# Performance work log

Hardware: AMD Instinct MI355X
Metric: run time of the kernel (lower is better)

## Reference

```python
import jax, jax.numpy as jnp
import numpy as np

L, D, DM, H, FF = 2048, 32, 1024, 16, 4096
DH = DM // H  # 64
SCALE = float(np.sqrt(DH))


def layernorm(x, g, b, eps=1e-5):
    mu = jnp.mean(x, axis=-1, keepdims=True)
    var = jnp.mean(jnp.square(x - mu), axis=-1, keepdims=True)
    return (x - mu) * jax.lax.rsqrt(var + eps) * g + b


def setup_inputs() -> dict:
    key = jax.random.key(0)
    ks = jax.random.split(key, 8)
    p = lambda k, shp: jax.random.normal(k, shp, jnp.float32) * 0.02
    return {
        "src": jax.random.normal(ks[0], (L, DM), jnp.float32),
        "target": jax.random.normal(ks[1], (L, D, DM), jnp.float32),
        "attn_mask": jnp.zeros((L, D), jnp.float32),
        "Wq": p(ks[2], (DM, DM)), "bq": jnp.zeros((DM,), jnp.float32),
        "Wk": p(ks[3], (DM, DM)), "bk": jnp.zeros((DM,), jnp.float32),
        "Wv": p(ks[4], (DM, DM)), "bv": jnp.zeros((DM,), jnp.float32),
        "W1": p(ks[5], (DM, FF)), "b1": jnp.zeros((FF,), jnp.float32),
        "W2": p(ks[6], (FF, DM)), "b2": jnp.zeros((DM,), jnp.float32),
        "g1": jnp.ones((DM,), jnp.float32), "beta1": jnp.zeros((DM,), jnp.float32),
        "g2": jnp.ones((DM,), jnp.float32), "beta2": jnp.zeros((DM,), jnp.float32),
    }


def reference(src, target, attn_mask, Wq, bq, Wk, bk, Wv, bv,
              W1, b1, W2, b2, g1, beta1, g2, beta2):
    # projections: src (L, DM), target (L, D, DM)
    q = (src @ Wq + bq).reshape(L, H, DH)            # (L, H, DH)
    k = (target @ Wk + bk).reshape(L, D, H, DH)       # (L, D, H, DH)
    v = (target @ Wv + bv).reshape(L, D, H, DH)
    # per-position attention over the D candidates: scores (H, L, D)
    scores = jnp.einsum('lhd,lkhd->hlk', q, k) / SCALE
    scores = scores + attn_mask[None, :, :]
    probs = jax.nn.softmax(scores, axis=-1)
    ctx = jnp.einsum('hlk,lkhd->lhd', probs, v).reshape(L, DM)
    x = layernorm(src + ctx, g1, beta1)
    ff = jax.nn.gelu(x @ W1 + b1, approximate=False) @ W2 + b2
    return layernorm(x + ff, g2, beta2)
```

## Files before the change

kernel.cpp:

```cpp
#include <hip/hip_runtime.h>
#include <hip/hip_bf16.h>

#define L  2048
#define D  32
#define DM 1024
#define H  16
#define DH 64
#define FF 4096

typedef unsigned short u16;
typedef __attribute__((ext_vector_type(8))) short bf16x8;
typedef __attribute__((ext_vector_type(4))) float f32x4;
typedef __attribute__((ext_vector_type(4))) unsigned int u32x4;
typedef __attribute__((ext_vector_type(8))) unsigned short u16x8;
typedef __attribute__((ext_vector_type(4))) unsigned short u16x4;

static __device__ __forceinline__ u16 f2bf(float f) {
    union { __hip_bfloat16 b; u16 u; } cv;
    cv.b = __float2bfloat16(f);
    return cv.u;
}
static __device__ __forceinline__ void gll16(const u16* gsrc, u16* ldst) {
    __builtin_amdgcn_global_load_lds(
        (const __attribute__((address_space(1))) unsigned int*)gsrc,
        (__attribute__((address_space(3))) unsigned int*)ldst, 16, 0, 0);
}

__global__ __launch_bounds__(256) void prep_bf(const float* __restrict__ a, u16* __restrict__ oa,
                                               const float* __restrict__ b, u16* __restrict__ ob) {
    const int i = blockIdx.x * 256 + threadIdx.x;
    const int na4 = (L * DM) / 4;
    const float* in;  u16* out;  int j;
    if (i < na4) { in = a; out = oa; j = i; }
    else         { in = b; out = ob; j = i - na4; }
    const float4 v = reinterpret_cast<const float4*>(in)[j];
    u16x4 o = { f2bf(v.x), f2bf(v.y), f2bf(v.z), f2bf(v.w) };
    *reinterpret_cast<u16x4*>(out + (long)j * 4) = o;
}

__global__ void prep_T(const float* __restrict__ Wq, u16* __restrict__ oWq,
                       const float* __restrict__ Wv, u16* __restrict__ oWv,
                       const float* __restrict__ W1, u16* __restrict__ oW1,
                       const float* __restrict__ W2, u16* __restrict__ oW2) {
    __shared__ float tile[32][33];
    const int b = blockIdx.x;
    const float* in; u16* out; int R, C, bx, by;
    if (b < 1024)      { in = Wq; out = oWq; R = DM; C = DM; int bb = b;        bx = (bb & 31) * 32;  by = (bb >> 5) * 32; }
    else if (b < 2048) { in = Wv; out = oWv; R = DM; C = DM; int bb = b - 1024; bx = (bb & 31) * 32;  by = (bb >> 5) * 32; }
    else if (b < 6144) { in = W1; out = oW1; R = DM; C = FF; int bb = b - 2048; bx = (bb & 127) * 32; by = (bb >> 7) * 32; }
    else               { in = W2; out = oW2; R = FF; C = DM; int bb = b - 6144; bx = (bb & 31) * 32;  by = (bb >> 5) * 32; }
    const int tx = threadIdx.x, ty = threadIdx.y;
    #pragma unroll
    for (int i = 0; i < 32; i += 8)
        tile[ty + i][tx] = in[(long)(by + ty + i) * C + bx + tx];
    __syncthreads();
    #pragma unroll
    for (int i = 0; i < 32; i += 8)
        out[(long)(bx + ty + i) * R + by + tx] = f2bf(tile[tx][ty + i]);
}

template<int EPI, int BN>
__global__ __launch_bounds__(256) void gemm128(
    const u16* __restrict__ A, int lda, long aZ,
    const u16* __restrict__ Bt, int ldb, long bZ,
    void* __restrict__ Cv, int ldc, long cZ,
    const float* __restrict__ bias, int biasZ, int K)
{
    constexpr int NI = BN / 32;
    __shared__ u16 As[128 * 64];
    __shared__ u16 Bs[BN * 64];
    const int t = threadIdx.x, lane = t & 63, w = t >> 6;
    const int z = blockIdx.z;
    const int nxy = gridDim.x * gridDim.y;
    int fid = blockIdx.y * gridDim.x + blockIdx.x;
    const int q8 = nxy >> 3;
    fid = (fid & 7) * q8 + (fid >> 3);
    const int bx = fid % gridDim.x, by = fid / gridDim.x;
    const int mBase = by * 128, nBase = bx * BN;
    const u16* Ab = A + (long)z * aZ;
    const u16* Bb = Bt + (long)z * bZ;
    const int wr = w >> 1, wc = w & 1;
    const int sr = lane >> 3, sg = lane & 7, sswz = sg ^ sr;
    f32x4 acc[4][NI];
    #pragma unroll
    for (int mi = 0; mi < 4; ++mi)
        #pragma unroll
        for (int ni = 0; ni < NI; ++ni) acc[mi][ni] = (f32x4){0.f, 0.f, 0.f, 0.f};

    for (int k0 = 0; k0 < K; k0 += 64) {
        #pragma unroll
        for (int i = 0; i < 4; ++i) {
            const int r = w * 32 + i * 8 + sr;
            gll16(&Ab[(long)(mBase + r) * lda + k0 + sswz * 8], &As[r * 64 + sg * 8]);
        }
        #pragma unroll
        for (int i = 0; i < NI; ++i) {
            const int r = w * (BN / 4) + i * 8 + sr;
            gll16(&Bb[(long)(nBase + r) * ldb + k0 + sswz * 8], &Bs[r * 64 + sg * 8]);
        }
        __syncthreads();
        #pragma unroll
        for (int ks = 0; ks < 2; ++ks) {
            bf16x8 aF[4], bF[NI];
            #pragma unroll
            for (int mi = 0; mi < 4; ++mi) {
                const int rr = wr * 64 + mi * 16 + (lane & 15);
                aF[mi] = *reinterpret_cast<const bf16x8*>(
                    &As[rr * 64 + ((ks * 4 + (lane >> 4)) ^ (rr & 7)) * 8]);
            }
            #pragma unroll
            for (int ni = 0; ni < NI; ++ni) {
                const int rr = wc * (BN / 2) + ni * 16 + (lane & 15);
                bF[ni] = *reinterpret_cast<const bf16x8*>(
                    &Bs[rr * 64 + ((ks * 4 + (lane >> 4)) ^ (rr & 7)) * 8]);
            }
            #pragma unroll
            for (int mi = 0; mi < 4; ++mi)
                #pragma unroll
                for (int ni = 0; ni < NI; ++ni)
                    acc[mi][ni] = __builtin_amdgcn_mfma_f32_16x16x32_bf16(
                        aF[mi], bF[ni], acc[mi][ni], 0, 0, 0);
        }
        __syncthreads();
    }
    const int rb = mBase + wr * 64 + ((lane >> 4) << 2);
    const int cb = nBase + wc * (BN / 2) + (lane & 15);
    #pragma unroll
    for (int mi = 0; mi < 4; ++mi) {
        #pragma unroll
        for (int ni = 0; ni < NI; ++ni) {
            const int col = cb + ni * 16;
            const float badd = bias ? bias[(long)z * biasZ + col] : 0.f;
            #pragma unroll
            for (int i = 0; i < 4; ++i) {
                float v = acc[mi][ni][i] + badd;
                if (EPI == 2) v = 0.5f * v * (1.f + erff(v * 0.70710678118654752f));
                const long off = (long)z * cZ + (long)(rb + mi * 16 + i) * ldc + col;
                if (EPI == 1) reinterpret_cast<float*>(Cv)[off] = v;
                else          reinterpret_cast<u16*>(Cv)[off]  = f2bf(v);
            }
        }
    }
}

#define NLV5 8
__global__ __launch_bounds__(512, 2) void attn_v5(
    const u16* __restrict__ qk,
    const float* __restrict__ target,
    const float* __restrict__ mask,
    u16* __restrict__ tw)
{
    extern __shared__ u16 smem[];
    u16*   tgtS0 = smem;
    u16*   tgtS1 = smem + D * DM;
    f32x4* red   = (f32x4*)(smem + 2 * D * DM);

    const int t = threadIdx.x, lane = t & 63, w = t >> 6;
    const int g = lane >> 4, hm = lane & 15;
    const int l0 = blockIdx.x * NLV5;

    float4 pf[16];
    bf16x8 qc[2][4];
    {
        const float* tl = target + (long)l0 * (D * DM);
        #pragma unroll
        for (int it = 0; it < 16; ++it)
            pf[it] = reinterpret_cast<const float4*>(tl)[it * 512 + t];
        #pragma unroll
        for (int it = 0; it < 16; ++it) {
            const int i = it * 512 + t;
            const int d = i >> 8, mm = (i & 255) * 4, cc = mm ^ ((d & 15) << 3);
            u16x4 o = { f2bf(pf[it].x), f2bf(pf[it].y), f2bf(pf[it].z), f2bf(pf[it].w) };
            *reinterpret_cast<u16x4*>(&tgtS0[d * DM + cc]) = o;
        }
        const float* tn = target + (long)(l0 + 1) * (D * DM);
        #pragma unroll
        for (int it = 0; it < 16; ++it)
            pf[it] = reinterpret_cast<const float4*>(tn)[it * 512 + t];
        const u16* qb = qk + (long)l0 * (H * DM) + hm * DM + w * 128 + g * 8;
        #pragma unroll
        for (int ks = 0; ks < 4; ++ks)
            qc[0][ks] = *reinterpret_cast<const bf16x8*>(&qb[ks * 32]);
    }
    __syncthreads();

    #pragma unroll
    for (int li = 0; li < NLV5; ++li) {
        const int l = l0 + li;
        const int cur = li & 1, nxt = cur ^ 1;
        u16* curS = cur ? tgtS1 : tgtS0;
        u16* nxtS = cur ? tgtS0 : tgtS1;

        const float* mrow = mask + (long)l * D;
        float mk[8];
        #pragma unroll
        for (int r = 0; r < 4; ++r) { mk[r] = mrow[4 * g + r]; mk[4 + r] = mrow[16 + 4 * g + r]; }

        if (li < NLV5 - 1) {
            #pragma unroll
            for (int it = 0; it < 16; ++it) {
                const int i = it * 512 + t;
                const int d = i >> 8, mm = (i & 255) * 4, cc = mm ^ ((d & 15) << 3);
                u16x4 o = { f2bf(pf[it].x), f2bf(pf[it].y), f2bf(pf[it].z), f2bf(pf[it].w) };
                *reinterpret_cast<u16x4*>(&nxtS[d * DM + cc]) = o;
            }
            if (li < NLV5 - 2) {
                const float* tn = target + (long)(l + 2) * (D * DM);
                #pragma unroll
                for (int it = 0; it < 16; ++it)
                    pf[it] = reinterpret_cast<const float4*>(tn)[it * 512 + t];
            }
            const u16* qn = qk + (long)(l + 1) * (H * DM) + hm * DM + w * 128 + g * 8;
            #pragma unroll
            for (int ks = 0; ks < 4; ++ks)
                qc[nxt][ks] = *reinterpret_cast<const bf16x8*>(&qn[ks * 32]);
        }

        f32x4 a0 = {0.f, 0.f, 0.f, 0.f}, a1 = {0.f, 0.f, 0.f, 0.f};
        const int swz = hm << 3;
        #pragma unroll
        for (int ks = 0; ks < 4; ++ks) {
            const int mcol = w * 128 + ks * 32 + g * 8;
            const bf16x8 x0 = *reinterpret_cast<const bf16x8*>(&curS[hm * DM + (mcol ^ swz)]);
            const bf16x8 x1 = *reinterpret_cast<const bf16x8*>(&curS[(16 + hm) * DM + (mcol ^ swz)]);
            a0 = __builtin_amdgcn_mfma_f32_16x16x32_bf16(x0, qc[cur][ks], a0, 0, 0, 0);
            a1 = __builtin_amdgcn_mfma_f32_16x16x32_bf16(x1, qc[cur][ks], a1, 0, 0, 0);
        }
        red[(w * 2 + 0) * 64 + lane] = a0;
        red[(w * 2 + 1) * 64 + lane] = a1;
        __syncthreads();

        f32x4 s0 = red[lane], s1 = red[64 + lane];
        #pragma unroll
        for (int ww = 1; ww < 8; ++ww) {
            s0 += red[(ww * 2 + 0) * 64 + lane];
            s1 += red[(ww * 2 + 1) * 64 + lane];
        }

        float sc[8];
        #pragma unroll
        for (int r = 0; r < 4; ++r) {
            sc[r]     = s0[r] * 0.125f + mk[r];
            sc[4 + r] = s1[r] * 0.125f + mk[4 + r];
        }
        float mx = sc[0];
        #pragma unroll
        for (int r = 1; r < 8; ++r) mx = fmaxf(mx, sc[r]);
        mx = fmaxf(mx, __shfl_xor(mx, 16));
        mx = fmaxf(mx, __shfl_xor(mx, 32));
        float sum = 0.f;
        #pragma unroll
        for (int r = 0; r < 8; ++r) { sc[r] = __expf(sc[r] - mx); sum += sc[r]; }
        sum += __shfl_xor(sum, 16);
        sum += __shfl_xor(sum, 32);
        const float pinv = 1.0f / sum;
        bf16x8 pfrag;
        #pragma unroll
        for (int r = 0; r < 8; ++r) pfrag[r] = (short)f2bf(sc[r] * pinv);

        u16* twl = tw + (long)l * (H * DM);
        const f32x4 zero = {0.f, 0.f, 0.f, 0.f};
        #pragma unroll
        for (int i = 0; i < 8; ++i) {
            const int mg = w * 8 + i;
            const int m = mg * 16 + hm;
            bf16x8 af;
            #pragma unroll
            for (int j = 0; j < 4; ++j) {
                const int d0 = 4 * g + j;
                const int d1 = 16 + 4 * g + j;
                af[j]     = (short)curS[d0 * DM + (m ^ (d0 << 3))];
                af[4 + j] = (short)curS[d1 * DM + (m ^ (d0 << 3))];
            }
            const f32x4 c = __builtin_amdgcn_mfma_f32_16x16x32_bf16(af, pfrag, zero, 0, 0, 0);
            u16x4 o = { f2bf(c[0]), f2bf(c[1]), f2bf(c[2]), f2bf(c[3]) };
            *reinterpret_cast<u16x4*>(&twl[hm * DM + mg * 16 + 4 * g]) = o;
        }
        __syncthreads();
    }
}

__global__ __launch_bounds__(256) void ln_fuse(
    const float* __restrict__ a, const float* __restrict__ zb, int nz, long zstride,
    const float* __restrict__ bvec,
    const float* __restrict__ g, const float* __restrict__ be,
    float* __restrict__ o32, u16* __restrict__ o16)
{
    const int l = blockIdx.x, t = threadIdx.x;
    __shared__ float S[4], SS[4];
    __shared__ float stats[2];
    const float4 va = reinterpret_cast<const float4*>(a + (long)l * DM)[t];
    float v[4] = { va.x, va.y, va.z, va.w };
    for (int zi = 0; zi < nz; ++zi) {
        const float4 q = reinterpret_cast<const float4*>(zb + (long)zi * zstride + (long)l * DM)[t];
        v[0] += q.x; v[1] += q.y; v[2] += q.z; v[3] += q.w;
    }
    if (bvec) {
        const float4 vv = reinterpret_cast<const float4*>(bvec)[t];
        v[0] += vv.x; v[1] += vv.y; v[2] += vv.z; v[3] += vv.w;
    }
    float s  = v[0] + v[1] + v[2] + v[3];
    float ss = v[0]*v[0] + v[1]*v[1] + v[2]*v[2] + v[3]*v[3];
    #pragma unroll
    for (int off = 32; off; off >>= 1) { s += __shfl_down(s, off); ss += __shfl_down(ss, off); }
    if ((t & 63) == 0) { S[t >> 6] = s; SS[t >> 6] = ss; }
    __syncthreads();
    if (t == 0) {
        const float St  = S[0] + S[1] + S[2] + S[3];
        const float SSt = SS[0] + SS[1] + SS[2] + SS[3];
        const float mu  = St * (1.f / DM);
        const float var = fmaxf(SSt * (1.f / DM) - mu * mu, 0.f);
        stats[0] = mu;
        stats[1] = rsqrtf(var + 1e-5f);
    }
    __syncthreads();
    const float mu = stats[0], rs = stats[1];
    const int c0 = t * 4;
    float ov[4];
    #pragma unroll
    for (int j = 0; j < 4; ++j) ov[j] = (v[j] - mu) * rs * g[c0 + j] + be[c0 + j];
    float4 o; o.x = ov[0]; o.y = ov[1]; o.z = ov[2]; o.w = ov[3];
    reinterpret_cast<float4*>(o32 + (long)l * DM)[t] = o;
    if (o16) {
        u16x4 q = { f2bf(ov[0]), f2bf(ov[1]), f2bf(ov[2]), f2bf(ov[3]) };
        *reinterpret_cast<u16x4*>(o16 + (long)l * DM + c0) = q;
    }
}

extern "C" void kernel_launch(void* const* d_in, const int* in_sizes, int n_in,
                              void* d_out, int out_size, void* d_ws, size_t ws_size,
                              hipStream_t stream)
{
    const float* src    = (const float*)d_in[0];
    const float* target = (const float*)d_in[1];
    const float* amask  = (const float*)d_in[2];
    const float* Wq = (const float*)d_in[3];
    const float* bq = (const float*)d_in[4];
    const float* Wk = (const float*)d_in[5];
    const float* Wv = (const float*)d_in[7];
    const float* bv = (const float*)d_in[8];
    const float* W1 = (const float*)d_in[9];
    const float* b1 = (const float*)d_in[10];
    const float* W2 = (const float*)d_in[11];
    const float* b2 = (const float*)d_in[12];
    const float* g1  = (const float*)d_in[13];
    const float* be1 = (const float*)d_in[14];
    const float* g2  = (const float*)d_in[15];
    const float* be2 = (const float*)d_in[16];

    char* ws = (char*)d_ws;
    const size_t MB = (size_t)1 << 20;
    u16*   src16 = (u16*)  (ws +  0 * MB);
    u16*   Wk16  = (u16*)  (ws +  4 * MB);
    u16*   WqT   = (u16*)  (ws +  6 * MB);
    u16*   WvT   = (u16*)  (ws +  8 * MB);
    u16*   W1T   = (u16*)  (ws + 10 * MB);
    u16*   W2T   = (u16*)  (ws + 18 * MB);
    u16*   Q16   = (u16*)  (ws + 26 * MB);
    u16*   qk16  = (u16*)  (ws + 30 * MB);
    u16*   Y16   = (u16*)  (ws + 30 * MB);
    float* ctx32 = (float*)(ws + 54 * MB);
    float* x32   = (float*)(ws + 62 * MB);
    u16*   x16   = (u16*)  (ws + 70 * MB);
    u16*   tw16  = (u16*)  (ws + 94 * MB);
    float* Z32   = (float*)(ws + 94 * MB);

    prep_bf<<<3072, 256, 0, stream>>>(src, src16, Wk, Wk16);
    prep_T<<<10240, dim3(32, 8), 0, stream>>>(Wq, WqT, Wv, WvT, W1, W1T, W2, W2T);

    gemm128<0, 64><<<dim3(DM / 64, L / 128, 1), 256, 0, stream>>>(
        src16, DM, 0, WqT, DM, 0, Q16, DM, 0, bq, 0, DM);
    gemm128<0, 128><<<dim3(DM / 128, L / 128, H), 256, 0, stream>>>(
        Q16, DM, DH, Wk16, DM, DH, qk16, H * DM, DM, nullptr, 0, DH);

    (void)hipFuncSetAttribute(reinterpret_cast<const void*>(&attn_v5),
                              hipFuncAttributeMaxDynamicSharedMemorySize, 144 * 1024);
    attn_v5<<<L / NLV5, 512, 144 * 1024, stream>>>(qk16, target, amask, tw16);

    gemm128<1, 64><<<dim3(1, L / 128, H), 256, 0, stream>>>(
        tw16, H * DM, DM, WvT, DM, (long)DH * DM, ctx32, DM, DH, bv, DH, DM);
    ln_fuse<<<L, 256, 0, stream>>>(src, ctx32, 1, 0, nullptr, g1, be1, x32, x16);
    gemm128<2, 128><<<dim3(FF / 128, L / 128, 1), 256, 0, stream>>>(
        x16, DM, 0, W1T, DM, 0, Y16, FF, 0, b1, 0, DM);
    gemm128<1, 128><<<dim3(DM / 128, L / 128, 4), 256, 0, stream>>>(
        Y16, FF, 1024, W2T, FF, 1024, Z32, DM, (long)L * DM, nullptr, 0, 1024);
    ln_fuse<<<L, 256, 0, stream>>>(x32, Z32, 4, (long)L * DM, b2, g2, be2, (float*)d_out, nullptr);
}
```

Measured before the change: 250.8 us.

## Double-buffer GEMM LDS tiles, add MFMA priority, merge prep kernels

Adds an optional double-buffered LDS path to the bf16 GEMM. The next K tile is loaded via global_load_lds while the current tile feeds MFMAs, so one barrier per iteration replaces two. It also raises wave priority around the MFMA block and fuses the two weight/activation conversion kernels into one launch. The price is doubled LDS per block, which may lower occupancy. The pipelined path relies on a single barrier to order the async LDS writes against reads of the other buffer.

```diff
diff --git a/kernel.cpp b/kernel.cpp
--- a/kernel.cpp
+++ b/kernel.cpp
@@ -26,30 +26,33 @@
         (__attribute__((address_space(3))) unsigned int*)ldst, 16, 0, 0);
 }
 
-__global__ __launch_bounds__(256) void prep_bf(const float* __restrict__ a, u16* __restrict__ oa,
-                                               const float* __restrict__ b, u16* __restrict__ ob) {
-    const int i = blockIdx.x * 256 + threadIdx.x;
-    const int na4 = (L * DM) / 4;
-    const float* in;  u16* out;  int j;
-    if (i < na4) { in = a; out = oa; j = i; }
-    else         { in = b; out = ob; j = i - na4; }
-    const float4 v = reinterpret_cast<const float4*>(in)[j];
-    u16x4 o = { f2bf(v.x), f2bf(v.y), f2bf(v.z), f2bf(v.w) };
-    *reinterpret_cast<u16x4*>(out + (long)j * 4) = o;
-}
-
-__global__ void prep_T(const float* __restrict__ Wq, u16* __restrict__ oWq,
-                       const float* __restrict__ Wv, u16* __restrict__ oWv,
-                       const float* __restrict__ W1, u16* __restrict__ oW1,
-                       const float* __restrict__ W2, u16* __restrict__ oW2) {
+__global__ __launch_bounds__(256) void prep_all(
+    const float* __restrict__ src, u16* __restrict__ osrc,
+    const float* __restrict__ Wk,  u16* __restrict__ oWk,
+    const float* __restrict__ Wq,  u16* __restrict__ oWq,
+    const float* __restrict__ Wv,  u16* __restrict__ oWv,
+    const float* __restrict__ W1,  u16* __restrict__ oW1,
+    const float* __restrict__ W2,  u16* __restrict__ oW2)
+{
+    const int b = blockIdx.x, t = threadIdx.x;
+    if (b >= 10240) {
+        const int i = (b - 10240) * 256 + t;
+        const int na4 = (L * DM) / 4;
+        const float* in;  u16* out;  int j;
+        if (i < na4) { in = src; out = osrc; j = i; }
+        else         { in = Wk;  out = oWk;  j = i - na4; }
+        const float4 v = reinterpret_cast<const float4*>(in)[j];
+        u16x4 o = { f2bf(v.x), f2bf(v.y), f2bf(v.z), f2bf(v.w) };
+        *reinterpret_cast<u16x4*>(out + (long)j * 4) = o;
+        return;
+    }
     __shared__ float tile[32][33];
-    const int b = blockIdx.x;
     const float* in; u16* out; int R, C, bx, by;
     if (b < 1024)      { in = Wq; out = oWq; R = DM; C = DM; int bb = b;        bx = (bb & 31) * 32;  by = (bb >> 5) * 32; }
     else if (b < 2048) { in = Wv; out = oWv; R = DM; C = DM; int bb = b - 1024; bx = (bb & 31) * 32;  by = (bb >> 5) * 32; }
     else if (b < 6144) { in = W1; out = oW1; R = DM; C = FF; int bb = b - 2048; bx = (bb & 127) * 32; by = (bb >> 7) * 32; }
     else               { in = W2; out = oW2; R = FF; C = DM; int bb = b - 6144; bx = (bb & 31) * 32;  by = (bb >> 5) * 32; }
-    const int tx = threadIdx.x, ty = threadIdx.y;
+    const int tx = t & 31, ty = t >> 5;
     #pragma unroll
     for (int i = 0; i < 32; i += 8)
         tile[ty + i][tx] = in[(long)(by + ty + i) * C + bx + tx];
@@ -59,7 +62,7 @@
         out[(long)(bx + ty + i) * R + by + tx] = f2bf(tile[tx][ty + i]);
 }
 
-template<int EPI, int BN>
+template<int EPI, int BN, int PIPE>
 __global__ __launch_bounds__(256) void gemm128(
     const u16* __restrict__ A, int lda, long aZ,
     const u16* __restrict__ Bt, int ldb, long bZ,
@@ -67,8 +70,9 @@
     const float* __restrict__ bias, int biasZ, int K)
 {
     constexpr int NI = BN / 32;
-    __shared__ u16 As[128 * 64];
-    __shared__ u16 Bs[BN * 64];
+    constexpr int ASZ = 128 * 64, BSZ = BN * 64;
+    __shared__ u16 As[(PIPE ? 2 : 1) * ASZ];
+    __shared__ u16 Bs[(PIPE ? 2 : 1) * BSZ];
     const int t = threadIdx.x, lane = t & 63, w = t >> 6;
     const int z = blockIdx.z;
     const int nxy = gridDim.x * gridDim.y;
@@ -87,18 +91,34 @@
         #pragma unroll
         for (int ni = 0; ni < NI; ++ni) acc[mi][ni] = (f32x4){0.f, 0.f, 0.f, 0.f};
 
-    for (int k0 = 0; k0 < K; k0 += 64) {
+    auto STAGE = [&](int buf, int k0) {
+        u16* Ad = As + buf * ASZ;
+        u16* Bd = Bs + buf * BSZ;
         #pragma unroll
         for (int i = 0; i < 4; ++i) {
             const int r = w * 32 + i * 8 + sr;
-            gll16(&Ab[(long)(mBase + r) * lda + k0 + sswz * 8], &As[r * 64 + sg * 8]);
+            gll16(&Ab[(long)(mBase + r) * lda + k0 + sswz * 8], &Ad[r * 64 + sg * 8]);
         }
         #pragma unroll
         for (int i = 0; i < NI; ++i) {
             const int r = w * (BN / 4) + i * 8 + sr;
-            gll16(&Bb[(long)(nBase + r) * ldb + k0 + sswz * 8], &Bs[r * 64 + sg * 8]);
-        }
-        __syncthreads();
+            gll16(&Bb[(long)(nBase + r) * ldb + k0 + sswz * 8], &Bd[r * 64 + sg * 8]);
+        }
+    };
+
+    if (PIPE) { STAGE(0, 0); }
+    int cur = 0;
+    for (int k0 = 0; k0 < K; k0 += 64) {
+        if (!PIPE) {
+            STAGE(0, k0);
+            __syncthreads();
+        } else {
+            __syncthreads();
+            if (k0 + 64 < K) STAGE(cur ^ 1, k0 + 64);
+        }
+        const u16* Ar = As + cur * ASZ;
+        const u16* Br = Bs + cur * BSZ;
+        __builtin_amdgcn_s_setprio(1);
         #pragma unroll
         for (int ks = 0; ks < 2; ++ks) {
             bf16x8 aF[4], bF[NI];
@@ -106,13 +126,13 @@
             for (int mi = 0; mi < 4; ++mi) {
                 const int rr = wr * 64 + mi * 16 + (lane & 15);
                 aF[mi] = *reinterpret_cast<const bf16x8*>(
-                    &As[rr * 64 + ((ks * 4 + (lane >> 4)) ^ (rr & 7)) * 8]);
+                    &Ar[rr * 64 + ((ks * 4 + (lane >> 4)) ^ (rr & 7)) * 8]);
             }
             #pragma unroll
             for (int ni = 0; ni < NI; ++ni) {
                 const int rr = wc * (BN / 2) + ni * 16 + (lane & 15);
                 bF[ni] = *reinterpret_cast<const bf16x8*>(
-                    &Bs[rr * 64 + ((ks * 4 + (lane >> 4)) ^ (rr & 7)) * 8]);
+                    &Br[rr * 64 + ((ks * 4 + (lane >> 4)) ^ (rr & 7)) * 8]);
             }
             #pragma unroll
             for (int mi = 0; mi < 4; ++mi)
@@ -121,7 +141,9 @@
                     acc[mi][ni] = __builtin_amdgcn_mfma_f32_16x16x32_bf16(
                         aF[mi], bF[ni], acc[mi][ni], 0, 0, 0);
         }
-        __syncthreads();
+        __builtin_amdgcn_s_setprio(0);
+        if (!PIPE) __syncthreads();
+        if (PIPE) cur ^= 1;
     }
     const int rb = mBase + wr * 64 + ((lane >> 4) << 2);
     const int cb = nBase + wc * (BN / 2) + (lane & 15);
@@ -365,24 +387,24 @@
     u16*   tw16  = (u16*)  (ws + 94 * MB);
     float* Z32   = (float*)(ws + 94 * MB);
 
-    prep_bf<<<3072, 256, 0, stream>>>(src, src16, Wk, Wk16);
-    prep_T<<<10240, dim3(32, 8), 0, stream>>>(Wq, WqT, Wv, WvT, W1, W1T, W2, W2T);
-
-    gemm128<0, 64><<<dim3(DM / 64, L / 128, 1), 256, 0, stream>>>(
+    prep_all<<<13312, 256, 0, stream>>>(src, src16, Wk, Wk16,
+                                        Wq, WqT, Wv, WvT, W1, W1T, W2, W2T);
+
+    gemm128<0, 64, 1><<<dim3(DM / 64, L / 128, 1), 256, 0, stream>>>(
         src16, DM, 0, WqT, DM, 0, Q16, DM, 0, bq, 0, DM);
-    gemm128<0, 128><<<dim3(DM / 128, L / 128, H), 256, 0, stream>>>(
+    gemm128<0, 128, 0><<<dim3(DM / 128, L / 128, H), 256, 0, stream>>>(
         Q16, DM, DH, Wk16, DM, DH, qk16, H * DM, DM, nullptr, 0, DH);
 
     (void)hipFuncSetAttribute(reinterpret_cast<const void*>(&attn_v5),
                               hipFuncAttributeMaxDynamicSharedMemorySize, 144 * 1024);
     attn_v5<<<L / NLV5, 512, 144 * 1024, stream>>>(qk16, target, amask, tw16);
 
-    gemm128<1, 64><<<dim3(1, L / 128, H), 256, 0, stream>>>(
+    gemm128<1, 64, 1><<<dim3(1, L / 128, H), 256, 0, stream>>>(
         tw16, H * DM, DM, WvT, DM, (long)DH * DM, ctx32, DM, DH, bv, DH, DM);
     ln_fuse<<<L, 256, 0, stream>>>(src, ctx32, 1, 0, nullptr, g1, be1, x32, x16);
-    gemm128<2, 128><<<dim3(FF / 128, L / 128, 1), 256, 0, stream>>>(
+    gemm128<2, 128, 1><<<dim3(FF / 128, L / 128, 1), 256, 0, stream>>>(
         x16, DM, 0, W1T, DM, 0, Y16, FF, 0, b1, 0, DM);
-    gemm128<1, 128><<<dim3(DM / 128, L / 128, 4), 256, 0, stream>>>(
+    gemm128<1, 128, 1><<<dim3(DM / 128, L / 128, 4), 256, 0, stream>>>(
         Y16, FF, 1024, W2T, FF, 1024, Z32, DM, (long)L * DM, nullptr, 0, 1024);
     ln_fuse<<<L, 256, 0, stream>>>(x32, Z32, 4, (long)L * DM, b2, g2, be2, (float*)d_out, nullptr);
 }
```

Result: faster. 242.7 us, median of 2 (-3.2%).
